# Optimization experiments

Measured on AMD Instinct MI355X. Metric: run time of the kernel, lower is better.

Reference implementation:

```python
import jax, jax.numpy as jnp
import numpy as np


def setup_inputs() -> dict:
    key = jax.random.key(0)
    k1, k2, k3, k4 = jax.random.split(key, 4)
    B, N, F_in, F_out = 8, 2048, 256, 256
    inp = jax.random.normal(k1, (B, N, F_in), dtype=jnp.float32)
    adj = jax.random.uniform(k2, (B, N, N), dtype=jnp.float32)
    stdv = 1.0 / np.sqrt(F_out)
    weight = jax.random.uniform(k3, (F_in, F_out), dtype=jnp.float32, minval=-stdv, maxval=stdv)
    bias = jax.random.uniform(k4, (F_out,), dtype=jnp.float32, minval=-stdv, maxval=stdv)
    return {"input": inp, "adj": adj, "weight": weight, "bias": bias}


def reference(input, adj, weight, bias):
    # d = (sum over dim 1 of adj) ** -0.5, matching torch adj.sum(dim=1)
    d = adj.sum(axis=1) ** -0.5  # [B, N]
    # D @ A @ D with diagonal D -> row/col broadcast scaling (same math)
    adj_norm = d[:, :, None] * adj * d[:, None, :]  # [B, N, N]
    support = jnp.einsum('bnf,fo->bno', input, weight)  # [B, N, F_out]
    output = jnp.einsum('bnm,bmo->bno', adj_norm, support) + bias
    return output
```

## Files before the change

kernel.cpp:

```cpp
#include <hip/hip_runtime.h>
#include <hip/hip_bf16.h>

#define BATCH 8
#define NDIM 2048
#define FDIM 256
#define CH 32

typedef float f32x4 __attribute__((ext_vector_type(4)));
typedef short bf16x8 __attribute__((ext_vector_type(8)));
typedef short bf16x4 __attribute__((ext_vector_type(4)));

__device__ __forceinline__ short f2bf(float f) {
  __hip_bfloat16 h = __float2bfloat16(f);
  short s;
  __builtin_memcpy(&s, &h, 2);
  return s;
}

__device__ __forceinline__ void gload_lds16(const void* g, void* l) {
  __builtin_amdgcn_global_load_lds(
      (const __attribute__((address_space(1))) void*)g,
      (__attribute__((address_space(3))) void*)l, 16, 0, 0);
}

__device__ __forceinline__ int aswz(int c, int r) {
  return 2 * ((c >> 1) ^ (r & 7)) + ((c & 1) ^ ((r >> 3) & 1));
}

__global__ __launch_bounds__(256) void k_colsum(const float* __restrict__ adj,
                                                float* __restrict__ part,
                                                const float* __restrict__ w,
                                                short* __restrict__ wt) {
  int bid = blockIdx.x;
  int t = threadIdx.x;
  if (bid < 512) {
    int cb = bid & 1;
    int ch = (bid >> 1) & (CH - 1);
    int b = bid >> 6;
    int col = cb * 1024 + t * 4;
    const float* p = adj + (size_t)b * NDIM * NDIM + (size_t)(ch * 64) * NDIM + col;
    f32x4 acc = {0.f, 0.f, 0.f, 0.f};
#pragma unroll 8
    for (int i = 0; i < 64; ++i) acc += *(const f32x4*)(p + (size_t)i * NDIM);
    *(f32x4*)(part + (size_t)(b * CH + ch) * NDIM + col) = acc;
  } else {
    __shared__ float tile[64][65];
    int bb = bid - 512;
    int bx = bb & 3, by = bb >> 2;
    int f0 = by * 64, o0 = bx * 64;
    int c4 = 4 * (t & 15);
#pragma unroll
    for (int q = 0; q < 4; ++q) {
      int r = (t >> 4) + 16 * q;
      f32x4 v = *(const f32x4*)(w + (size_t)(f0 + r) * FDIM + o0 + c4);
#pragma unroll
      for (int i = 0; i < 4; ++i) tile[r][c4 + i] = v[i];
    }
    __syncthreads();
#pragma unroll
    for (int q = 0; q < 4; ++q) {
      int r = (t >> 4) + 16 * q;
      bf16x4 pk;
#pragma unroll
      for (int i = 0; i < 4; ++i) pk[i] = f2bf(tile[c4 + i][r]);
      *(bf16x4*)(wt + (size_t)(o0 + r) * FDIM + f0 + c4) = pk;
    }
  }
}

__global__ __launch_bounds__(512) void k_support(const float* __restrict__ in,
                                                 const short* __restrict__ wt,
                                                 const float* __restrict__ part,
                                                 float* __restrict__ dnorm,
                                                 short* __restrict__ st) {
  __shared__ float Alf[3][64 * 64];
  __shared__ short Bl[3][256 * 64];
  __shared__ float dnLds[64];
  int t = threadIdx.x, lane = t & 63, w = t >> 6;
  int wm = w & 1, wn = w >> 1;
  int b = blockIdx.x & 7;
  int m0 = (blockIdx.x >> 3) * 64;
  const float* inb = in + ((size_t)b * NDIM + m0) * FDIM;

  if (t < 64) {
    float s = 0.f;
#pragma unroll
    for (int c = 0; c < CH; ++c) s += part[(size_t)(b * CH + c) * NDIM + m0 + t];
    float dv = rsqrtf(s);
    dnLds[t] = dv;
    dnorm[b * NDIM + m0 + t] = dv;
  }
  asm volatile("s_waitcnt vmcnt(0)" ::: "memory");

  int s0 = t, s1 = 512 + t;
  int r0 = s0 >> 4, c0 = aswz(s0 & 15, r0);
  int r1 = s1 >> 4, c1 = aswz(s1 & 15, r1);
  const float* a0s = inb + (size_t)r0 * FDIM + c0 * 4;
  const float* a1s = inb + (size_t)r1 * FDIM + c1 * 4;
  int arow = t >> 3;
  int schk = (t & 7) ^ (arow & 7);
  const short* bsrc = wt + (size_t)arow * FDIM + 8 * schk;

  f32x4 acc[2][4];
#pragma unroll
  for (int m = 0; m < 2; ++m)
#pragma unroll
    for (int n = 0; n < 4; ++n) acc[m][n] = {0.f, 0.f, 0.f, 0.f};

  int lr = lane & 15, kg = lane >> 4, sw = lane & 7;
  int bA = (lr >> 3) & 1;

  auto stage = [&](int k, int bp) {
    size_t ko = (size_t)k * 64;
    gload_lds16(a0s + ko, &Alf[bp][s0 * 4]);
    gload_lds16(a1s + ko, &Alf[bp][s1 * 4]);
#pragma unroll
    for (int i = 0; i < 4; ++i)
      gload_lds16(bsrc + (size_t)(i * 64) * FDIM + ko, &Bl[bp][(i * 512 + t) * 8]);
  };

  auto body = [&](int it, int bc, int bp, int mode) {
    if (mode == 0) {
      stage(it + 2, bp);
      asm volatile("s_waitcnt vmcnt(12)" ::: "memory");
    } else if (mode == 1) {
      asm volatile("s_waitcnt vmcnt(6)" ::: "memory");
    } else {
      asm volatile("s_waitcnt vmcnt(0)" ::: "memory");
    }
    __builtin_amdgcn_s_barrier();
    asm volatile("" ::: "memory");
    __builtin_amdgcn_sched_barrier(0);
#pragma unroll
    for (int h = 0; h < 2; ++h) {
      int gk = h * 4 + kg;
      int p2 = 2 * (gk ^ sw);
      bf16x8 af[2];
#pragma unroll
      for (int mf = 0; mf < 2; ++mf) {
        int row = wm * 32 + mf * 16 + lr;
        f32x4 lo = *(const f32x4*)&Alf[bc][row * 64 + (p2 + bA) * 4];
        f32x4 hi = *(const f32x4*)&Alf[bc][row * 64 + (p2 + (bA ^ 1)) * 4];
#pragma unroll
        for (int j = 0; j < 4; ++j) { af[mf][j] = f2bf(lo[j]); af[mf][4 + j] = f2bf(hi[j]); }
      }
      int kc = (gk ^ sw) * 8;
      bf16x8 bv0 = *(const bf16x8*)&Bl[bc][(wn * 64 + lr) * 64 + kc];
      bf16x8 bv1 = *(const bf16x8*)&Bl[bc][(wn * 64 + 16 + lr) * 64 + kc];
      bf16x8 bv2 = *(const bf16x8*)&Bl[bc][(wn * 64 + 32 + lr) * 64 + kc];
      bf16x8 bv3 = *(const bf16x8*)&Bl[bc][(wn * 64 + 48 + lr) * 64 + kc];
      acc[0][0] = __builtin_amdgcn_mfma_f32_16x16x32_bf16(af[0], bv0, acc[0][0], 0, 0, 0);
      acc[0][1] = __builtin_amdgcn_mfma_f32_16x16x32_bf16(af[0], bv1, acc[0][1], 0, 0, 0);
      acc[0][2] = __builtin_amdgcn_mfma_f32_16x16x32_bf16(af[0], bv2, acc[0][2], 0, 0, 0);
      acc[0][3] = __builtin_amdgcn_mfma_f32_16x16x32_bf16(af[0], bv3, acc[0][3], 0, 0, 0);
      acc[1][0] = __builtin_amdgcn_mfma_f32_16x16x32_bf16(af[1], bv0, acc[1][0], 0, 0, 0);
      acc[1][1] = __builtin_amdgcn_mfma_f32_16x16x32_bf16(af[1], bv1, acc[1][1], 0, 0, 0);
      acc[1][2] = __builtin_amdgcn_mfma_f32_16x16x32_bf16(af[1], bv2, acc[1][2], 0, 0, 0);
      acc[1][3] = __builtin_amdgcn_mfma_f32_16x16x32_bf16(af[1], bv3, acc[1][3], 0, 0, 0);
    }
    asm volatile("s_waitcnt lgkmcnt(0)" ::: "memory");
    __builtin_amdgcn_s_barrier();
    asm volatile("" ::: "memory");
  };

  stage(0, 0);
  stage(1, 1);
  body(0, 0, 2, 0);
  body(1, 1, 0, 0);
  body(2, 2, 1, 1);
  body(3, 0, 2, 2);

#pragma unroll
  for (int mf = 0; mf < 2; ++mf) {
    int rloc = wm * 32 + mf * 16 + kg * 4;
    int row = m0 + rloc;
    float dm[4];
#pragma unroll
    for (int j = 0; j < 4; ++j) dm[j] = dnLds[rloc + j];
#pragma unroll
    for (int nf = 0; nf < 4; ++nf) {
      int col = wn * 64 + nf * 16 + lr;
      bf16x4 pk;
#pragma unroll
      for (int j = 0; j < 4; ++j) pk[j] = f2bf(acc[mf][nf][j] * dm[j]);
      *(bf16x4*)(st + ((size_t)(b * FDIM + col)) * NDIM + row) = pk;
    }
  }
}

__global__ __launch_bounds__(512) void k_main(const float* __restrict__ adj,
                                              const short* __restrict__ st,
                                              const float* __restrict__ dnorm,
                                              const float* __restrict__ bias,
                                              float* __restrict__ out) {
  __shared__ float Alf[3][64 * 64];
  __shared__ short Bl[3][256 * 64];
  int t = threadIdx.x, lane = t & 63, w = t >> 6;
  int wm = w & 1, wn = w >> 1;
  int b = blockIdx.x & 7;
  int n0 = (blockIdx.x >> 3) * 64;
  const float* ab = adj + ((size_t)b * NDIM + n0) * NDIM;
  const short* stb = st + (size_t)b * FDIM * NDIM;

  int s0 = t, s1 = 512 + t;
  int r0 = s0 >> 4, c0 = aswz(s0 & 15, r0);
  int r1 = s1 >> 4, c1 = aswz(s1 & 15, r1);
  const float* a0s = ab + (size_t)r0 * NDIM + c0 * 4;
  const float* a1s = ab + (size_t)r1 * NDIM + c1 * 4;
  int arow = t >> 3;
  int schk = (t & 7) ^ (arow & 7);
  const short* bsrc = stb + (size_t)arow * NDIM + 8 * schk;

  f32x4 acc[2][4];
#pragma unroll
  for (int m = 0; m < 2; ++m)
#pragma unroll
    for (int n = 0; n < 4; ++n) acc[m][n] = {0.f, 0.f, 0.f, 0.f};

  int lr = lane & 15, kg = lane >> 4, sw = lane & 7;
  int bA = (lr >> 3) & 1;

  auto stage = [&](int k, int bp) {
    size_t ko = (size_t)k * 64;
    gload_lds16(a0s + ko, &Alf[bp][s0 * 4]);
    gload_lds16(a1s + ko, &Alf[bp][s1 * 4]);
#pragma unroll
    for (int i = 0; i < 4; ++i)
      gload_lds16(bsrc + (size_t)(i * 64) * NDIM + ko, &Bl[bp][(i * 512 + t) * 8]);
  };

  auto body = [&](int it, int bc, int bp, int mode) {
    if (mode == 0) {
      stage(it + 2, bp);
      asm volatile("s_waitcnt vmcnt(12)" ::: "memory");
    } else if (mode == 1) {
      asm volatile("s_waitcnt vmcnt(6)" ::: "memory");
    } else {
      asm volatile("s_waitcnt vmcnt(0)" ::: "memory");
    }
    __builtin_amdgcn_s_barrier();
    asm volatile("" ::: "memory");
    __builtin_amdgcn_sched_barrier(0);
#pragma unroll
    for (int h = 0; h < 2; ++h) {
      int gk = h * 4 + kg;
      int p2 = 2 * (gk ^ sw);
      bf16x8 af[2];
#pragma unroll
      for (int mf = 0; mf < 2; ++mf) {
        int row = wm * 32 + mf * 16 + lr;
        f32x4 lo = *(const f32x4*)&Alf[bc][row * 64 + (p2 + bA) * 4];
        f32x4 hi = *(const f32x4*)&Alf[bc][row * 64 + (p2 + (bA ^ 1)) * 4];
#pragma unroll
        for (int j = 0; j < 4; ++j) { af[mf][j] = f2bf(lo[j]); af[mf][4 + j] = f2bf(hi[j]); }
      }
      int kc = (gk ^ sw) * 8;
      bf16x8 bv0 = *(const bf16x8*)&Bl[bc][(wn * 64 + lr) * 64 + kc];
      bf16x8 bv1 = *(const bf16x8*)&Bl[bc][(wn * 64 + 16 + lr) * 64 + kc];
      bf16x8 bv2 = *(const bf16x8*)&Bl[bc][(wn * 64 + 32 + lr) * 64 + kc];
      bf16x8 bv3 = *(const bf16x8*)&Bl[bc][(wn * 64 + 48 + lr) * 64 + kc];
      acc[0][0] = __builtin_amdgcn_mfma_f32_16x16x32_bf16(af[0], bv0, acc[0][0], 0, 0, 0);
      acc[0][1] = __builtin_amdgcn_mfma_f32_16x16x32_bf16(af[0], bv1, acc[0][1], 0, 0, 0);
      acc[0][2] = __builtin_amdgcn_mfma_f32_16x16x32_bf16(af[0], bv2, acc[0][2], 0, 0, 0);
      acc[0][3] = __builtin_amdgcn_mfma_f32_16x16x32_bf16(af[0], bv3, acc[0][3], 0, 0, 0);
      acc[1][0] = __builtin_amdgcn_mfma_f32_16x16x32_bf16(af[1], bv0, acc[1][0], 0, 0, 0);
      acc[1][1] = __builtin_amdgcn_mfma_f32_16x16x32_bf16(af[1], bv1, acc[1][1], 0, 0, 0);
      acc[1][2] = __builtin_amdgcn_mfma_f32_16x16x32_bf16(af[1], bv2, acc[1][2], 0, 0, 0);
      acc[1][3] = __builtin_amdgcn_mfma_f32_16x16x32_bf16(af[1], bv3, acc[1][3], 0, 0, 0);
    }
    asm volatile("s_waitcnt lgkmcnt(0)" ::: "memory");
    __builtin_amdgcn_s_barrier();
    asm volatile("" ::: "memory");
  };

  stage(0, 0);
  stage(1, 1);
  for (int itb = 0; itb < 30; itb += 3) {
    body(itb + 0, 0, 2, 0);
    body(itb + 1, 1, 0, 0);
    body(itb + 2, 2, 1, 0);
  }
  body(30, 0, 2, 1);
  body(31, 1, 0, 2);

#pragma unroll
  for (int mf = 0; mf < 2; ++mf) {
    int row = n0 + wm * 32 + mf * 16 + kg * 4;
    f32x4 dr = *(const f32x4*)&dnorm[b * NDIM + row];
#pragma unroll
    for (int nf = 0; nf < 4; ++nf) {
      int col = wn * 64 + nf * 16 + lr;
      float bv = bias[col];
      float* op = out + ((size_t)b * NDIM + row) * FDIM + col;
#pragma unroll
      for (int j = 0; j < 4; ++j) op[(size_t)j * FDIM] = dr[j] * acc[mf][nf][j] + bv;
    }
  }
}

extern "C" void kernel_launch(void* const* d_in, const int* in_sizes, int n_in,
                              void* d_out, int out_size, void* d_ws, size_t ws_size,
                              hipStream_t stream) {
  (void)in_sizes; (void)n_in; (void)out_size; (void)ws_size;
  const float* input = (const float*)d_in[0];
  const float* adj = (const float*)d_in[1];
  const float* weight = (const float*)d_in[2];
  const float* bias = (const float*)d_in[3];
  float* out = (float*)d_out;

  char* ws = (char*)d_ws;
  short* st = (short*)ws;
  float* dnorm = (float*)(ws + 8ull * 1024 * 1024);
  float* part = (float*)(ws + 8ull * 1024 * 1024 + 65536);
  short* wt = (short*)(ws + 8ull * 1024 * 1024 + 65536 + 2ull * 1024 * 1024);

  k_colsum<<<dim3(528), dim3(256), 0, stream>>>(adj, part, weight, wt);
  k_support<<<dim3(BATCH * (NDIM / 64)), dim3(512), 0, stream>>>(input, wt, part, dnorm, st);
  k_main<<<dim3(BATCH * (NDIM / 64)), dim3(512), 0, stream>>>(adj, st, dnorm, bias, out);
}
```

Measured before the change: 70.48 us.

## Fuse column-sum, support GEMM and main GEMM into one kernel with per-batch barriers

The column-sum, support GEMM and main GEMM launches are merged into one 256-block kernel. A small init kernel transposes the weight and resets the counters. Each block first column-sums its own 64 rows of adj, then waits at an atomic-counter barrier per batch. It then computes its 64-row support tile and waits at a second barrier before running the main adj×support GEMM, keeping the degree normalisation in LDS. This removes launch gaps and the global dnorm round trip, and the colsum read of adj may warm caches for the main pass. In exchange, correctness depends on all 256 blocks being resident at once, and blocks spin while waiting.

```diff
diff --git a/kernel.cpp b/kernel.cpp
--- a/kernel.cpp
+++ b/kernel.cpp
@@ -27,52 +27,44 @@
   return 2 * ((c >> 1) ^ (r & 7)) + ((c & 1) ^ ((r >> 3) & 1));
 }
 
-__global__ __launch_bounds__(256) void k_colsum(const float* __restrict__ adj,
-                                                float* __restrict__ part,
-                                                const float* __restrict__ w,
-                                                short* __restrict__ wt) {
-  int bid = blockIdx.x;
+__global__ __launch_bounds__(256) void k_init(const float* __restrict__ w,
+                                              short* __restrict__ wt,
+                                              unsigned* __restrict__ ctr) {
   int t = threadIdx.x;
-  if (bid < 512) {
-    int cb = bid & 1;
-    int ch = (bid >> 1) & (CH - 1);
-    int b = bid >> 6;
-    int col = cb * 1024 + t * 4;
-    const float* p = adj + (size_t)b * NDIM * NDIM + (size_t)(ch * 64) * NDIM + col;
-    f32x4 acc = {0.f, 0.f, 0.f, 0.f};
-#pragma unroll 8
-    for (int i = 0; i < 64; ++i) acc += *(const f32x4*)(p + (size_t)i * NDIM);
-    *(f32x4*)(part + (size_t)(b * CH + ch) * NDIM + col) = acc;
-  } else {
-    __shared__ float tile[64][65];
-    int bb = bid - 512;
-    int bx = bb & 3, by = bb >> 2;
-    int f0 = by * 64, o0 = bx * 64;
-    int c4 = 4 * (t & 15);
-#pragma unroll
-    for (int q = 0; q < 4; ++q) {
-      int r = (t >> 4) + 16 * q;
-      f32x4 v = *(const f32x4*)(w + (size_t)(f0 + r) * FDIM + o0 + c4);
-#pragma unroll
-      for (int i = 0; i < 4; ++i) tile[r][c4 + i] = v[i];
-    }
-    __syncthreads();
-#pragma unroll
-    for (int q = 0; q < 4; ++q) {
-      int r = (t >> 4) + 16 * q;
-      bf16x4 pk;
-#pragma unroll
-      for (int i = 0; i < 4; ++i) pk[i] = f2bf(tile[c4 + i][r]);
-      *(bf16x4*)(wt + (size_t)(o0 + r) * FDIM + f0 + c4) = pk;
-    }
-  }
-}
-
-__global__ __launch_bounds__(512) void k_support(const float* __restrict__ in,
-                                                 const short* __restrict__ wt,
-                                                 const float* __restrict__ part,
-                                                 float* __restrict__ dnorm,
-                                                 short* __restrict__ st) {
+  if (blockIdx.x == 0) {
+    if (t < 16) ctr[t] = 0u;
+    return;
+  }
+  __shared__ float tile[64][65];
+  int bb = blockIdx.x - 1;
+  int bx = bb & 3, by = bb >> 2;
+  int f0 = by * 64, o0 = bx * 64;
+  int c4 = 4 * (t & 15);
+#pragma unroll
+  for (int q = 0; q < 4; ++q) {
+    int r = (t >> 4) + 16 * q;
+    f32x4 v = *(const f32x4*)(w + (size_t)(f0 + r) * FDIM + o0 + c4);
+#pragma unroll
+    for (int i = 0; i < 4; ++i) tile[r][c4 + i] = v[i];
+  }
+  __syncthreads();
+#pragma unroll
+  for (int q = 0; q < 4; ++q) {
+    int r = (t >> 4) + 16 * q;
+    bf16x4 pk;
+#pragma unroll
+    for (int i = 0; i < 4; ++i) pk[i] = f2bf(tile[c4 + i][r]);
+    *(bf16x4*)(wt + (size_t)(o0 + r) * FDIM + f0 + c4) = pk;
+  }
+}
+
+__global__ __launch_bounds__(512) void k_fused(const float* __restrict__ adj,
+                                               const float* __restrict__ in,
+                                               const short* __restrict__ wt,
+                                               float* __restrict__ part,
+                                               const float* __restrict__ bias,
+                                               float* __restrict__ out,
+                                               unsigned* __restrict__ ctr) {
   __shared__ float Alf[3][64 * 64];
   __shared__ short Bl[3][256 * 64];
   __shared__ float dnLds[64];
@@ -80,220 +72,232 @@
   int wm = w & 1, wn = w >> 1;
   int b = blockIdx.x & 7;
   int m0 = (blockIdx.x >> 3) * 64;
-  const float* inb = in + ((size_t)b * NDIM + m0) * FDIM;
-
-  if (t < 64) {
-    float s = 0.f;
-#pragma unroll
-    for (int c = 0; c < CH; ++c) s += part[(size_t)(b * CH + c) * NDIM + m0 + t];
-    float dv = rsqrtf(s);
-    dnLds[t] = dv;
-    dnorm[b * NDIM + m0 + t] = dv;
-  }
-  asm volatile("s_waitcnt vmcnt(0)" ::: "memory");
-
+  unsigned* ctrA = ctr;
+  unsigned* ctrB = ctr + 8;
+
+  {
+    int col = t * 4;
+    const float* p = adj + (size_t)b * NDIM * NDIM + (size_t)m0 * NDIM + col;
+    f32x4 acc = {0.f, 0.f, 0.f, 0.f};
+#pragma unroll 8
+    for (int i = 0; i < 64; ++i) acc += *(const f32x4*)(p + (size_t)i * NDIM);
+    *(f32x4*)(part + (size_t)(b * CH + (m0 >> 6)) * NDIM + col) = acc;
+  }
+  __threadfence();
+  __syncthreads();
+  if (t == 0) {
+    __hip_atomic_fetch_add(&ctrA[b], 1u, __ATOMIC_ACQ_REL, __HIP_MEMORY_SCOPE_AGENT);
+    while (__hip_atomic_load(&ctrA[b], __ATOMIC_ACQUIRE, __HIP_MEMORY_SCOPE_AGENT) < 32u)
+      __builtin_amdgcn_s_sleep(4);
+  }
+  __syncthreads();
+  __threadfence();
+
+  int lr = lane & 15, kg = lane >> 4, sw = lane & 7;
+  int bA = (lr >> 3) & 1;
   int s0 = t, s1 = 512 + t;
   int r0 = s0 >> 4, c0 = aswz(s0 & 15, r0);
   int r1 = s1 >> 4, c1 = aswz(s1 & 15, r1);
-  const float* a0s = inb + (size_t)r0 * FDIM + c0 * 4;
-  const float* a1s = inb + (size_t)r1 * FDIM + c1 * 4;
   int arow = t >> 3;
   int schk = (t & 7) ^ (arow & 7);
-  const short* bsrc = wt + (size_t)arow * FDIM + 8 * schk;
-
-  f32x4 acc[2][4];
-#pragma unroll
-  for (int m = 0; m < 2; ++m)
-#pragma unroll
-    for (int n = 0; n < 4; ++n) acc[m][n] = {0.f, 0.f, 0.f, 0.f};
-
-  int lr = lane & 15, kg = lane >> 4, sw = lane & 7;
-  int bA = (lr >> 3) & 1;
-
-  auto stage = [&](int k, int bp) {
-    size_t ko = (size_t)k * 64;
-    gload_lds16(a0s + ko, &Alf[bp][s0 * 4]);
-    gload_lds16(a1s + ko, &Alf[bp][s1 * 4]);
-#pragma unroll
-    for (int i = 0; i < 4; ++i)
-      gload_lds16(bsrc + (size_t)(i * 64) * FDIM + ko, &Bl[bp][(i * 512 + t) * 8]);
-  };
-
-  auto body = [&](int it, int bc, int bp, int mode) {
-    if (mode == 0) {
-      stage(it + 2, bp);
-      asm volatile("s_waitcnt vmcnt(12)" ::: "memory");
-    } else if (mode == 1) {
-      asm volatile("s_waitcnt vmcnt(6)" ::: "memory");
-    } else {
-      asm volatile("s_waitcnt vmcnt(0)" ::: "memory");
+
+  {
+    if (t < 64) {
+      float s = 0.f;
+#pragma unroll
+      for (int c = 0; c < CH; ++c) s += part[(size_t)(b * CH + c) * NDIM + m0 + t];
+      dnLds[t] = rsqrtf(s);
     }
-    __builtin_amdgcn_s_barrier();
-    asm volatile("" ::: "memory");
-    __builtin_amdgcn_sched_barrier(0);
-#pragma unroll
-    for (int h = 0; h < 2; ++h) {
-      int gk = h * 4 + kg;
-      int p2 = 2 * (gk ^ sw);
-      bf16x8 af[2];
-#pragma unroll
-      for (int mf = 0; mf < 2; ++mf) {
-        int row = wm * 32 + mf * 16 + lr;
-        f32x4 lo = *(const f32x4*)&Alf[bc][row * 64 + (p2 + bA) * 4];
-        f32x4 hi = *(const f32x4*)&Alf[bc][row * 64 + (p2 + (bA ^ 1)) * 4];
-#pragma unroll
-        for (int j = 0; j < 4; ++j) { af[mf][j] = f2bf(lo[j]); af[mf][4 + j] = f2bf(hi[j]); }
-      }
-      int kc = (gk ^ sw) * 8;
-      bf16x8 bv0 = *(const bf16x8*)&Bl[bc][(wn * 64 + lr) * 64 + kc];
-      bf16x8 bv1 = *(const bf16x8*)&Bl[bc][(wn * 64 + 16 + lr) * 64 + kc];
-      bf16x8 bv2 = *(const bf16x8*)&Bl[bc][(wn * 64 + 32 + lr) * 64 + kc];
-      bf16x8 bv3 = *(const bf16x8*)&Bl[bc][(wn * 64 + 48 + lr) * 64 + kc];
-      acc[0][0] = __builtin_amdgcn_mfma_f32_16x16x32_bf16(af[0], bv0, acc[0][0], 0, 0, 0);
-      acc[0][1] = __builtin_amdgcn_mfma_f32_16x16x32_bf16(af[0], bv1, acc[0][1], 0, 0, 0);
-      acc[0][2] = __builtin_amdgcn_mfma_f32_16x16x32_bf16(af[0], bv2, acc[0][2], 0, 0, 0);
-      acc[0][3] = __builtin_amdgcn_mfma_f32_16x16x32_bf16(af[0], bv3, acc[0][3], 0, 0, 0);
-      acc[1][0] = __builtin_amdgcn_mfma_f32_16x16x32_bf16(af[1], bv0, acc[1][0], 0, 0, 0);
-      acc[1][1] = __builtin_amdgcn_mfma_f32_16x16x32_bf16(af[1], bv1, acc[1][1], 0, 0, 0);
-      acc[1][2] = __builtin_amdgcn_mfma_f32_16x16x32_bf16(af[1], bv2, acc[1][2], 0, 0, 0);
-      acc[1][3] = __builtin_amdgcn_mfma_f32_16x16x32_bf16(af[1], bv3, acc[1][3], 0, 0, 0);
+    asm volatile("s_waitcnt vmcnt(0)" ::: "memory");
+
+    const float* inb = in + ((size_t)b * NDIM + m0) * FDIM;
+    const float* a0s = inb + (size_t)r0 * FDIM + c0 * 4;
+    const float* a1s = inb + (size_t)r1 * FDIM + c1 * 4;
+    const short* bsrc = wt + (size_t)arow * FDIM + 8 * schk;
+    short* st = (short*)nullptr;
+    st = (short*)((char*)part - (8ull * 1024 * 1024 + 65536));
+
+    f32x4 acc[2][4];
+#pragma unroll
+    for (int m = 0; m < 2; ++m)
+#pragma unroll
+      for (int n = 0; n < 4; ++n) acc[m][n] = {0.f, 0.f, 0.f, 0.f};
+
+    auto stage = [&](int k, int bp) {
+      size_t ko = (size_t)k * 64;
+      gload_lds16(a0s + ko, &Alf[bp][s0 * 4]);
+      gload_lds16(a1s + ko, &Alf[bp][s1 * 4]);
+#pragma unroll
+      for (int i = 0; i < 4; ++i)
+        gload_lds16(bsrc + (size_t)(i * 64) * FDIM + ko, &Bl[bp][(i * 512 + t) * 8]);
+    };
+    auto body = [&](int bc, int bp, int mode, int itp2) {
+      if (mode == 0) {
+        stage(itp2, bp);
+        asm volatile("s_waitcnt vmcnt(12)" ::: "memory");
+      } else if (mode == 1) {
+        asm volatile("s_waitcnt vmcnt(6)" ::: "memory");
+      } else {
+        asm volatile("s_waitcnt vmcnt(0)" ::: "memory");
+      }
+      __builtin_amdgcn_s_barrier();
+      asm volatile("" ::: "memory");
+      __builtin_amdgcn_sched_barrier(0);
+#pragma unroll
+      for (int h = 0; h < 2; ++h) {
+        int gk = h * 4 + kg;
+        int p2 = 2 * (gk ^ sw);
+        bf16x8 af[2];
+#pragma unroll
+        for (int mf = 0; mf < 2; ++mf) {
+          int row = wm * 32 + mf * 16 + lr;
+          f32x4 lo = *(const f32x4*)&Alf[bc][row * 64 + (p2 + bA) * 4];
+          f32x4 hi = *(const f32x4*)&Alf[bc][row * 64 + (p2 + (bA ^ 1)) * 4];
+#pragma unroll
+          for (int j = 0; j < 4; ++j) { af[mf][j] = f2bf(lo[j]); af[mf][4 + j] = f2bf(hi[j]); }
+        }
+        int kc = (gk ^ sw) * 8;
+        bf16x8 bv0 = *(const bf16x8*)&Bl[bc][(wn * 64 + lr) * 64 + kc];
+        bf16x8 bv1 = *(const bf16x8*)&Bl[bc][(wn * 64 + 16 + lr) * 64 + kc];
+        bf16x8 bv2 = *(const bf16x8*)&Bl[bc][(wn * 64 + 32 + lr) * 64 + kc];
+        bf16x8 bv3 = *(const bf16x8*)&Bl[bc][(wn * 64 + 48 + lr) * 64 + kc];
+        acc[0][0] = __builtin_amdgcn_mfma_f32_16x16x32_bf16(af[0], bv0, acc[0][0], 0, 0, 0);
+        acc[0][1] = __builtin_amdgcn_mfma_f32_16x16x32_bf16(af[0], bv1, acc[0][1], 0, 0, 0);
+        acc[0][2] = __builtin_amdgcn_mfma_f32_16x16x32_bf16(af[0], bv2, acc[0][2], 0, 0, 0);
+        acc[0][3] = __builtin_amdgcn_mfma_f32_16x16x32_bf16(af[0], bv3, acc[0][3], 0, 0, 0);
+        acc[1][0] = __builtin_amdgcn_mfma_f32_16x16x32_bf16(af[1], bv0, acc[1][0], 0, 0, 0);
+        acc[1][1] = __builtin_amdgcn_mfma_f32_16x16x32_bf16(af[1], bv1, acc[1][1], 0, 0, 0);
+        acc[1][2] = __builtin_amdgcn_mfma_f32_16x16x32_bf16(af[1], bv2, acc[1][2], 0, 0, 0);
+        acc[1][3] = __builtin_amdgcn_mfma_f32_16x16x32_bf16(af[1], bv3, acc[1][3], 0, 0, 0);
+      }
+      asm volatile("s_waitcnt lgkmcnt(0)" ::: "memory");
+      __builtin_amdgcn_s_barrier();
+      asm volatile("" ::: "memory");
+    };
+
+    stage(0, 0);
+    stage(1, 1);
+    body(0, 2, 0, 2);
+    body(1, 0, 0, 3);
+    body(2, 1, 1, 0);
+    body(0, 2, 2, 0);
+
+#pragma unroll
+    for (int mf = 0; mf < 2; ++mf) {
+      int rloc = wm * 32 + mf * 16 + kg * 4;
+      int row = m0 + rloc;
+      float dm[4];
+#pragma unroll
+      for (int j = 0; j < 4; ++j) dm[j] = dnLds[rloc + j];
+#pragma unroll
+      for (int nf = 0; nf < 4; ++nf) {
+        int col = wn * 64 + nf * 16 + lr;
+        bf16x4 pk;
+#pragma unroll
+        for (int j = 0; j < 4; ++j) pk[j] = f2bf(acc[mf][nf][j] * dm[j]);
+        *(bf16x4*)(st + ((size_t)(b * FDIM + col)) * NDIM + row) = pk;
+      }
     }
-    asm volatile("s_waitcnt lgkmcnt(0)" ::: "memory");
-    __builtin_amdgcn_s_barrier();
-    asm volatile("" ::: "memory");
-  };
-
-  stage(0, 0);
-  stage(1, 1);
-  body(0, 0, 2, 0);
-  body(1, 1, 0, 0);
-  body(2, 2, 1, 1);
-  body(3, 0, 2, 2);
-
-#pragma unroll
-  for (int mf = 0; mf < 2; ++mf) {
-    int rloc = wm * 32 + mf * 16 + kg * 4;
-    int row = m0 + rloc;
-    float dm[4];
-#pragma unroll
-    for (int j = 0; j < 4; ++j) dm[j] = dnLds[rloc + j];
-#pragma unroll
-    for (int nf = 0; nf < 4; ++nf) {
-      int col = wn * 64 + nf * 16 + lr;
-      bf16x4 pk;
-#pragma unroll
-      for (int j = 0; j < 4; ++j) pk[j] = f2bf(acc[mf][nf][j] * dm[j]);
-      *(bf16x4*)(st + ((size_t)(b * FDIM + col)) * NDIM + row) = pk;
+  }
+  __threadfence();
+  __syncthreads();
+  if (t == 0) {
+    __hip_atomic_fetch_add(&ctrB[b], 1u, __ATOMIC_ACQ_REL, __HIP_MEMORY_SCOPE_AGENT);
+    while (__hip_atomic_load(&ctrB[b], __ATOMIC_ACQUIRE, __HIP_MEMORY_SCOPE_AGENT) < 32u)
+      __builtin_amdgcn_s_sleep(4);
+  }
+  __syncthreads();
+  __threadfence();
+
+  {
+    const short* st = (const short*)((char*)part - (8ull * 1024 * 1024 + 65536));
+    const float* ab = adj + ((size_t)b * NDIM + m0) * NDIM;
+    const short* stb = st + (size_t)b * FDIM * NDIM;
+    const float* a0s = ab + (size_t)r0 * NDIM + c0 * 4;
+    const float* a1s = ab + (size_t)r1 * NDIM + c1 * 4;
+    const short* bsrc = stb + (size_t)arow * NDIM + 8 * schk;
+
+    f32x4 acc[2][4];
+#pragma unroll
+    for (int m = 0; m < 2; ++m)
+#pragma unroll
+      for (int n = 0; n < 4; ++n) acc[m][n] = {0.f, 0.f, 0.f, 0.f};
+
+    auto stage = [&](int k, int bp) {
+      size_t ko = (size_t)k * 64;
+      gload_lds16(a0s + ko, &Alf[bp][s0 * 4]);
+      gload_lds16(a1s + ko, &Alf[bp][s1 * 4]);
+#pragma unroll
+      for (int i = 0; i < 4; ++i)
+        gload_lds16(bsrc + (size_t)(i * 64) * NDIM + ko, &Bl[bp][(i * 512 + t) * 8]);
+    };
+    auto body = [&](int it, int bc, int bp, int mode) {
+      if (mode == 0) {
+        stage(it + 2, bp);
+        asm volatile("s_waitcnt vmcnt(12)" ::: "memory");
+      } else if (mode == 1) {
+        asm volatile("s_waitcnt vmcnt(6)" ::: "memory");
+      } else {
+        asm volatile("s_waitcnt vmcnt(0)" ::: "memory");
+      }
+      __builtin_amdgcn_s_barrier();
+      asm volatile("" ::: "memory");
+      __builtin_amdgcn_sched_barrier(0);
+#pragma unroll
+      for (int h = 0; h < 2; ++h) {
+        int gk = h * 4 + kg;
+        int p2 = 2 * (gk ^ sw);
+        bf16x8 af[2];
+#pragma unroll
+        for (int mf = 0; mf < 2; ++mf) {
+          int row = wm * 32 + mf * 16 + lr;
+          f32x4 lo = *(const f32x4*)&Alf[bc][row * 64 + (p2 + bA) * 4];
+          f32x4 hi = *(const f32x4*)&Alf[bc][row * 64 + (p2 + (bA ^ 1)) * 4];
+#pragma unroll
+          for (int j = 0; j < 4; ++j) { af[mf][j] = f2bf(lo[j]); af[mf][4 + j] = f2bf(hi[j]); }
+        }
+        int kc = (gk ^ sw) * 8;
+        bf16x8 bv0 = *(const bf16x8*)&Bl[bc][(wn * 64 + lr) * 64 + kc];
+        bf16x8 bv1 = *(const bf16x8*)&Bl[bc][(wn * 64 + 16 + lr) * 64 + kc];
+        bf16x8 bv2 = *(const bf16x8*)&Bl[bc][(wn * 64 + 32 + lr) * 64 + kc];
+        bf16x8 bv3 = *(const bf16x8*)&Bl[bc][(wn * 64 + 48 + lr) * 64 + kc];
+        acc[0][0] = __builtin_amdgcn_mfma_f32_16x16x32_bf16(af[0], bv0, acc[0][0], 0, 0, 0);
+        acc[0][1] = __builtin_amdgcn_mfma_f32_16x16x32_bf16(af[0], bv1, acc[0][1], 0, 0, 0);
+        acc[0][2] = __builtin_amdgcn_mfma_f32_16x16x32_bf16(af[0], bv2, acc[0][2], 0, 0, 0);
+        acc[0][3] = __builtin_amdgcn_mfma_f32_16x16x32_bf16(af[0], bv3, acc[0][3], 0, 0, 0);
+        acc[1][0] = __builtin_amdgcn_mfma_f32_16x16x32_bf16(af[1], bv0, acc[1][0], 0, 0, 0);
+        acc[1][1] = __builtin_amdgcn_mfma_f32_16x16x32_bf16(af[1], bv1, acc[1][1], 0, 0, 0);
+        acc[1][2] = __builtin_amdgcn_mfma_f32_16x16x32_bf16(af[1], bv2, acc[1][2], 0, 0, 0);
+        acc[1][3] = __builtin_amdgcn_mfma_f32_16x16x32_bf16(af[1], bv3, acc[1][3], 0, 0, 0);
+      }
+      asm volatile("s_waitcnt lgkmcnt(0)" ::: "memory");
+      __builtin_amdgcn_s_barrier();
+      asm volatile("" ::: "memory");
+    };
+
+    stage(0, 0);
+    stage(1, 1);
+    for (int itb = 0; itb < 30; itb += 3) {
+      body(itb + 0, 0, 2, 0);
+      body(itb + 1, 1, 0, 0);
+      body(itb + 2, 2, 1, 0);
     }
-  }
-}
-
-__global__ __launch_bounds__(512) void k_main(const float* __restrict__ adj,
-                                              const short* __restrict__ st,
-                                              const float* __restrict__ dnorm,
-                                              const float* __restrict__ bias,
-                                              float* __restrict__ out) {
-  __shared__ float Alf[3][64 * 64];
-  __shared__ short Bl[3][256 * 64];
-  int t = threadIdx.x, lane = t & 63, w = t >> 6;
-  int wm = w & 1, wn = w >> 1;
-  int b = blockIdx.x & 7;
-  int n0 = (blockIdx.x >> 3) * 64;
-  const float* ab = adj + ((size_t)b * NDIM + n0) * NDIM;
-  const short* stb = st + (size_t)b * FDIM * NDIM;
-
-  int s0 = t, s1 = 512 + t;
-  int r0 = s0 >> 4, c0 = aswz(s0 & 15, r0);
-  int r1 = s1 >> 4, c1 = aswz(s1 & 15, r1);
-  const float* a0s = ab + (size_t)r0 * NDIM + c0 * 4;
-  const float* a1s = ab + (size_t)r1 * NDIM + c1 * 4;
-  int arow = t >> 3;
-  int schk = (t & 7) ^ (arow & 7);
-  const short* bsrc = stb + (size_t)arow * NDIM + 8 * schk;
-
-  f32x4 acc[2][4];
-#pragma unroll
-  for (int m = 0; m < 2; ++m)
-#pragma unroll
-    for (int n = 0; n < 4; ++n) acc[m][n] = {0.f, 0.f, 0.f, 0.f};
-
-  int lr = lane & 15, kg = lane >> 4, sw = lane & 7;
-  int bA = (lr >> 3) & 1;
-
-  auto stage = [&](int k, int bp) {
-    size_t ko = (size_t)k * 64;
-    gload_lds16(a0s + ko, &Alf[bp][s0 * 4]);
-    gload_lds16(a1s + ko, &Alf[bp][s1 * 4]);
-#pragma unroll
-    for (int i = 0; i < 4; ++i)
-      gload_lds16(bsrc + (size_t)(i * 64) * NDIM + ko, &Bl[bp][(i * 512 + t) * 8]);
-  };
-
-  auto body = [&](int it, int bc, int bp, int mode) {
-    if (mode == 0) {
-      stage(it + 2, bp);
-      asm volatile("s_waitcnt vmcnt(12)" ::: "memory");
-    } else if (mode == 1) {
-      asm volatile("s_waitcnt vmcnt(6)" ::: "memory");
-    } else {
-      asm volatile("s_waitcnt vmcnt(0)" ::: "memory");
-    }
-    __builtin_amdgcn_s_barrier();
-    asm volatile("" ::: "memory");
-    __builtin_amdgcn_sched_barrier(0);
-#pragma unroll
-    for (int h = 0; h < 2; ++h) {
-      int gk = h * 4 + kg;
-      int p2 = 2 * (gk ^ sw);
-      bf16x8 af[2];
-#pragma unroll
-      for (int mf = 0; mf < 2; ++mf) {
-        int row = wm * 32 + mf * 16 + lr;
-        f32x4 lo = *(const f32x4*)&Alf[bc][row * 64 + (p2 + bA) * 4];
-        f32x4 hi = *(const f32x4*)&Alf[bc][row * 64 + (p2 + (bA ^ 1)) * 4];
-#pragma unroll
-        for (int j = 0; j < 4; ++j) { af[mf][j] = f2bf(lo[j]); af[mf][4 + j] = f2bf(hi[j]); }
-      }
-      int kc = (gk ^ sw) * 8;
-      bf16x8 bv0 = *(const bf16x8*)&Bl[bc][(wn * 64 + lr) * 64 + kc];
-      bf16x8 bv1 = *(const bf16x8*)&Bl[bc][(wn * 64 + 16 + lr) * 64 + kc];
-      bf16x8 bv2 = *(const bf16x8*)&Bl[bc][(wn * 64 + 32 + lr) * 64 + kc];
-      bf16x8 bv3 = *(const bf16x8*)&Bl[bc][(wn * 64 + 48 + lr) * 64 + kc];
-      acc[0][0] = __builtin_amdgcn_mfma_f32_16x16x32_bf16(af[0], bv0, acc[0][0], 0, 0, 0);
-      acc[0][1] = __builtin_amdgcn_mfma_f32_16x16x32_bf16(af[0], bv1, acc[0][1], 0, 0, 0);
-      acc[0][2] = __builtin_amdgcn_mfma_f32_16x16x32_bf16(af[0], bv2, acc[0][2], 0, 0, 0);
-      acc[0][3] = __builtin_amdgcn_mfma_f32_16x16x32_bf16(af[0], bv3, acc[0][3], 0, 0, 0);
-      acc[1][0] = __builtin_amdgcn_mfma_f32_16x16x32_bf16(af[1], bv0, acc[1][0], 0, 0, 0);
-      acc[1][1] = __builtin_amdgcn_mfma_f32_16x16x32_bf16(af[1], bv1, acc[1][1], 0, 0, 0);
-      acc[1][2] = __builtin_amdgcn_mfma_f32_16x16x32_bf16(af[1], bv2, acc[1][2], 0, 0, 0);
-      acc[1][3] = __builtin_amdgcn_mfma_f32_16x16x32_bf16(af[1], bv3, acc[1][3], 0, 0, 0);
-    }
-    asm volatile("s_waitcnt lgkmcnt(0)" ::: "memory");
-    __builtin_amdgcn_s_barrier();
-    asm volatile("" ::: "memory");
-  };
-
-  stage(0, 0);
-  stage(1, 1);
-  for (int itb = 0; itb < 30; itb += 3) {
-    body(itb + 0, 0, 2, 0);
-    body(itb + 1, 1, 0, 0);
-    body(itb + 2, 2, 1, 0);
-  }
-  body(30, 0, 2, 1);
-  body(31, 1, 0, 2);
-
-#pragma unroll
-  for (int mf = 0; mf < 2; ++mf) {
-    int row = n0 + wm * 32 + mf * 16 + kg * 4;
-    f32x4 dr = *(const f32x4*)&dnorm[b * NDIM + row];
-#pragma unroll
-    for (int nf = 0; nf < 4; ++nf) {
-      int col = wn * 64 + nf * 16 + lr;
-      float bv = bias[col];
-      float* op = out + ((size_t)b * NDIM + row) * FDIM + col;
-#pragma unroll
-      for (int j = 0; j < 4; ++j) op[(size_t)j * FDIM] = dr[j] * acc[mf][nf][j] + bv;
+    body(30, 0, 2, 1);
+    body(31, 1, 0, 2);
+
+#pragma unroll
+    for (int mf = 0; mf < 2; ++mf) {
+      int rloc = wm * 32 + mf * 16 + kg * 4;
+      int row = m0 + rloc;
+      f32x4 dr = *(const f32x4*)&dnLds[rloc];
+#pragma unroll
+      for (int nf = 0; nf < 4; ++nf) {
+        int col = wn * 64 + nf * 16 + lr;
+        float bv = bias[col];
+        float* op = out + ((size_t)b * NDIM + row) * FDIM + col;
+#pragma unroll
+        for (int j = 0; j < 4; ++j) op[(size_t)j * FDIM] = dr[j] * acc[mf][nf][j] + bv;
+      }
     }
   }
 }
@@ -309,12 +313,10 @@
   float* out = (float*)d_out;
 
   char* ws = (char*)d_ws;
-  short* st = (short*)ws;
-  float* dnorm = (float*)(ws + 8ull * 1024 * 1024);
   float* part = (float*)(ws + 8ull * 1024 * 1024 + 65536);
   short* wt = (short*)(ws + 8ull * 1024 * 1024 + 65536 + 2ull * 1024 * 1024);
-
-  k_colsum<<<dim3(528), dim3(256), 0, stream>>>(adj, part, weight, wt);
-  k_support<<<dim3(BATCH * (NDIM / 64)), dim3(512), 0, stream>>>(input, wt, part, dnorm, st);
-  k_main<<<dim3(BATCH * (NDIM / 64)), dim3(512), 0, stream>>>(adj, st, dnorm, bias, out);
-}
+  unsigned* ctr = (unsigned*)(ws + 16ull * 1024 * 1024);
+
+  k_init<<<dim3(17), dim3(256), 0, stream>>>(weight, wt, ctr);
+  k_fused<<<dim3(256), dim3(512), 0, stream>>>(adj, input, wt, part, bias, out, ctr);
+}
```

Result: slower. 260.9 us (+270.2%).

## Fuse colsum, support GEMM and main GEMM into one cooperative persistent kernel

Applied to the files above, without the earlier changes.

Replaces the three-kernel sequence with a small init kernel (weight transpose plus counter reset) and a single cooperative kernel of 256 blocks. Each block computes its own column-sum partial, then its slice of the support GEMM, then its tile of the main GEMM, and uses per-batch atomic-counter barriers between phases instead of kernel boundaries. This removes launch gaps and tail effects between kernels, and the adj slab read for the colsum may still be in cache when the main phase reads it. It depends on every block being co-resident, relies on spin-wait barriers, and falls back to the old launches if the cooperative launch fails.

```diff
diff --git a/kernel.cpp b/kernel.cpp
--- a/kernel.cpp
+++ b/kernel.cpp
@@ -25,6 +25,279 @@
 
 __device__ __forceinline__ int aswz(int c, int r) {
   return 2 * ((c >> 1) ^ (r & 7)) + ((c & 1) ^ ((r >> 3) & 1));
+}
+
+__global__ __launch_bounds__(256) void k_init(const float* __restrict__ w,
+                                              short* __restrict__ wt,
+                                              unsigned* __restrict__ ctr) {
+  int t = threadIdx.x;
+  if (blockIdx.x == 0) {
+    for (int i = t; i < 512; i += 256) ctr[i] = 0u;
+    return;
+  }
+  __shared__ float tile[64][65];
+  int bb = blockIdx.x - 1;
+  int bx = bb & 3, by = bb >> 2;
+  int f0 = by * 64, o0 = bx * 64;
+  int c4 = 4 * (t & 15);
+#pragma unroll
+  for (int q = 0; q < 4; ++q) {
+    int r = (t >> 4) + 16 * q;
+    f32x4 v = *(const f32x4*)(w + (size_t)(f0 + r) * FDIM + o0 + c4);
+#pragma unroll
+    for (int i = 0; i < 4; ++i) tile[r][c4 + i] = v[i];
+  }
+  __syncthreads();
+#pragma unroll
+  for (int q = 0; q < 4; ++q) {
+    int r = (t >> 4) + 16 * q;
+    bf16x4 pk;
+#pragma unroll
+    for (int i = 0; i < 4; ++i) pk[i] = f2bf(tile[c4 + i][r]);
+    *(bf16x4*)(wt + (size_t)(o0 + r) * FDIM + f0 + c4) = pk;
+  }
+}
+
+__global__ __launch_bounds__(512) void k_fused(const float* __restrict__ adj,
+                                               const float* __restrict__ in,
+                                               const short* __restrict__ wt,
+                                               float* __restrict__ part,
+                                               short* __restrict__ st,
+                                               const float* __restrict__ bias,
+                                               float* __restrict__ out,
+                                               unsigned* __restrict__ ctr) {
+  __shared__ float Alf[3][64 * 64];
+  __shared__ short Bl[3][256 * 64];
+  __shared__ float dnLds[64];
+  int t = threadIdx.x, lane = t & 63, w = t >> 6;
+  int wm = w & 1, wn = w >> 1;
+  int b = blockIdx.x & 7;
+  int m0 = (blockIdx.x >> 3) * 64;
+
+  {
+    int col = t * 4;
+    const float* p = adj + (size_t)b * NDIM * NDIM + (size_t)m0 * NDIM + col;
+    f32x4 acc = {0.f, 0.f, 0.f, 0.f};
+#pragma unroll 8
+    for (int i = 0; i < 64; ++i) acc += *(const f32x4*)(p + (size_t)i * NDIM);
+    *(f32x4*)(part + (size_t)(b * CH + (m0 >> 6)) * NDIM + col) = acc;
+  }
+  __threadfence();
+  __syncthreads();
+  if (t == 0) {
+    unsigned* c = &ctr[b * 32];
+    __hip_atomic_fetch_add(c, 1u, __ATOMIC_ACQ_REL, __HIP_MEMORY_SCOPE_AGENT);
+    while (__hip_atomic_load(c, __ATOMIC_ACQUIRE, __HIP_MEMORY_SCOPE_AGENT) < 32u)
+      __builtin_amdgcn_s_sleep(16);
+  }
+  __syncthreads();
+  __threadfence();
+
+  int lr = lane & 15, kg = lane >> 4, sw = lane & 7;
+  int bA = (lr >> 3) & 1;
+  int s0 = t, s1 = 512 + t;
+  int r0 = s0 >> 4, c0 = aswz(s0 & 15, r0);
+  int r1 = s1 >> 4, c1 = aswz(s1 & 15, r1);
+  int arow = t >> 3;
+  int schk = (t & 7) ^ (arow & 7);
+
+  {
+    if (t < 64) {
+      float s = 0.f;
+#pragma unroll
+      for (int c = 0; c < CH; ++c) s += part[(size_t)(b * CH + c) * NDIM + m0 + t];
+      dnLds[t] = rsqrtf(s);
+    }
+    asm volatile("s_waitcnt vmcnt(0)" ::: "memory");
+
+    const float* inb = in + ((size_t)b * NDIM + m0) * FDIM;
+    const float* a0s = inb + (size_t)r0 * FDIM + c0 * 4;
+    const float* a1s = inb + (size_t)r1 * FDIM + c1 * 4;
+    const short* bsrc = wt + (size_t)arow * FDIM + 8 * schk;
+
+    f32x4 acc[2][4];
+#pragma unroll
+    for (int m = 0; m < 2; ++m)
+#pragma unroll
+      for (int n = 0; n < 4; ++n) acc[m][n] = {0.f, 0.f, 0.f, 0.f};
+
+    auto stage = [&](int k, int bp) {
+      size_t ko = (size_t)k * 64;
+      gload_lds16(a0s + ko, &Alf[bp][s0 * 4]);
+      gload_lds16(a1s + ko, &Alf[bp][s1 * 4]);
+#pragma unroll
+      for (int i = 0; i < 4; ++i)
+        gload_lds16(bsrc + (size_t)(i * 64) * FDIM + ko, &Bl[bp][(i * 512 + t) * 8]);
+    };
+    auto body = [&](int bc, int bp, int mode, int itp2) {
+      if (mode == 0) {
+        stage(itp2, bp);
+        asm volatile("s_waitcnt vmcnt(12)" ::: "memory");
+      } else if (mode == 1) {
+        asm volatile("s_waitcnt vmcnt(6)" ::: "memory");
+      } else {
+        asm volatile("s_waitcnt vmcnt(0)" ::: "memory");
+      }
+      __builtin_amdgcn_s_barrier();
+      asm volatile("" ::: "memory");
+      __builtin_amdgcn_sched_barrier(0);
+#pragma unroll
+      for (int h = 0; h < 2; ++h) {
+        int gk = h * 4 + kg;
+        int p2 = 2 * (gk ^ sw);
+        bf16x8 af[2];
+#pragma unroll
+        for (int mf = 0; mf < 2; ++mf) {
+          int row = wm * 32 + mf * 16 + lr;
+          f32x4 lo = *(const f32x4*)&Alf[bc][row * 64 + (p2 + bA) * 4];
+          f32x4 hi = *(const f32x4*)&Alf[bc][row * 64 + (p2 + (bA ^ 1)) * 4];
+#pragma unroll
+          for (int j = 0; j < 4; ++j) { af[mf][j] = f2bf(lo[j]); af[mf][4 + j] = f2bf(hi[j]); }
+        }
+        int kc = (gk ^ sw) * 8;
+        bf16x8 bv0 = *(const bf16x8*)&Bl[bc][(wn * 64 + lr) * 64 + kc];
+        bf16x8 bv1 = *(const bf16x8*)&Bl[bc][(wn * 64 + 16 + lr) * 64 + kc];
+        bf16x8 bv2 = *(const bf16x8*)&Bl[bc][(wn * 64 + 32 + lr) * 64 + kc];
+        bf16x8 bv3 = *(const bf16x8*)&Bl[bc][(wn * 64 + 48 + lr) * 64 + kc];
+        acc[0][0] = __builtin_amdgcn_mfma_f32_16x16x32_bf16(af[0], bv0, acc[0][0], 0, 0, 0);
+        acc[0][1] = __builtin_amdgcn_mfma_f32_16x16x32_bf16(af[0], bv1, acc[0][1], 0, 0, 0);
+        acc[0][2] = __builtin_amdgcn_mfma_f32_16x16x32_bf16(af[0], bv2, acc[0][2], 0, 0, 0);
+        acc[0][3] = __builtin_amdgcn_mfma_f32_16x16x32_bf16(af[0], bv3, acc[0][3], 0, 0, 0);
+        acc[1][0] = __builtin_amdgcn_mfma_f32_16x16x32_bf16(af[1], bv0, acc[1][0], 0, 0, 0);
+        acc[1][1] = __builtin_amdgcn_mfma_f32_16x16x32_bf16(af[1], bv1, acc[1][1], 0, 0, 0);
+        acc[1][2] = __builtin_amdgcn_mfma_f32_16x16x32_bf16(af[1], bv2, acc[1][2], 0, 0, 0);
+        acc[1][3] = __builtin_amdgcn_mfma_f32_16x16x32_bf16(af[1], bv3, acc[1][3], 0, 0, 0);
+      }
+      asm volatile("s_waitcnt lgkmcnt(0)" ::: "memory");
+      __builtin_amdgcn_s_barrier();
+      asm volatile("" ::: "memory");
+    };
+
+    stage(0, 0);
+    stage(1, 1);
+    body(0, 2, 0, 2);
+    body(1, 0, 0, 3);
+    body(2, 1, 1, 0);
+    body(0, 2, 2, 0);
+
+#pragma unroll
+    for (int mf = 0; mf < 2; ++mf) {
+      int rloc = wm * 32 + mf * 16 + kg * 4;
+      int row = m0 + rloc;
+      float dm[4];
+#pragma unroll
+      for (int j = 0; j < 4; ++j) dm[j] = dnLds[rloc + j];
+#pragma unroll
+      for (int nf = 0; nf < 4; ++nf) {
+        int col = wn * 64 + nf * 16 + lr;
+        bf16x4 pk;
+#pragma unroll
+        for (int j = 0; j < 4; ++j) pk[j] = f2bf(acc[mf][nf][j] * dm[j]);
+        *(bf16x4*)(st + ((size_t)(b * FDIM + col)) * NDIM + row) = pk;
+      }
+    }
+  }
+  __threadfence();
+  __syncthreads();
+  if (t == 0) {
+    unsigned* c = &ctr[256 + b * 32];
+    __hip_atomic_fetch_add(c, 1u, __ATOMIC_ACQ_REL, __HIP_MEMORY_SCOPE_AGENT);
+    while (__hip_atomic_load(c, __ATOMIC_ACQUIRE, __HIP_MEMORY_SCOPE_AGENT) < 32u)
+      __builtin_amdgcn_s_sleep(16);
+  }
+  __syncthreads();
+  __threadfence();
+
+  {
+    const float* ab = adj + ((size_t)b * NDIM + m0) * NDIM;
+    const short* stb = st + (size_t)b * FDIM * NDIM;
+    const float* a0s = ab + (size_t)r0 * NDIM + c0 * 4;
+    const float* a1s = ab + (size_t)r1 * NDIM + c1 * 4;
+    const short* bsrc = stb + (size_t)arow * NDIM + 8 * schk;
+
+    f32x4 acc[2][4];
+#pragma unroll
+    for (int m = 0; m < 2; ++m)
+#pragma unroll
+      for (int n = 0; n < 4; ++n) acc[m][n] = {0.f, 0.f, 0.f, 0.f};
+
+    auto stage = [&](int k, int bp) {
+      size_t ko = (size_t)k * 64;
+      gload_lds16(a0s + ko, &Alf[bp][s0 * 4]);
+      gload_lds16(a1s + ko, &Alf[bp][s1 * 4]);
+#pragma unroll
+      for (int i = 0; i < 4; ++i)
+        gload_lds16(bsrc + (size_t)(i * 64) * NDIM + ko, &Bl[bp][(i * 512 + t) * 8]);
+    };
+    auto body = [&](int it, int bc, int bp, int mode) {
+      if (mode == 0) {
+        stage(it + 2, bp);
+        asm volatile("s_waitcnt vmcnt(12)" ::: "memory");
+      } else if (mode == 1) {
+        asm volatile("s_waitcnt vmcnt(6)" ::: "memory");
+      } else {
+        asm volatile("s_waitcnt vmcnt(0)" ::: "memory");
+      }
+      __builtin_amdgcn_s_barrier();
+      asm volatile("" ::: "memory");
+      __builtin_amdgcn_sched_barrier(0);
+#pragma unroll
+      for (int h = 0; h < 2; ++h) {
+        int gk = h * 4 + kg;
+        int p2 = 2 * (gk ^ sw);
+        bf16x8 af[2];
+#pragma unroll
+        for (int mf = 0; mf < 2; ++mf) {
+          int row = wm * 32 + mf * 16 + lr;
+          f32x4 lo = *(const f32x4*)&Alf[bc][row * 64 + (p2 + bA) * 4];
+          f32x4 hi = *(const f32x4*)&Alf[bc][row * 64 + (p2 + (bA ^ 1)) * 4];
+#pragma unroll
+          for (int j = 0; j < 4; ++j) { af[mf][j] = f2bf(lo[j]); af[mf][4 + j] = f2bf(hi[j]); }
+        }
+        int kc = (gk ^ sw) * 8;
+        bf16x8 bv0 = *(const bf16x8*)&Bl[bc][(wn * 64 + lr) * 64 + kc];
+        bf16x8 bv1 = *(const bf16x8*)&Bl[bc][(wn * 64 + 16 + lr) * 64 + kc];
+        bf16x8 bv2 = *(const bf16x8*)&Bl[bc][(wn * 64 + 32 + lr) * 64 + kc];
+        bf16x8 bv3 = *(const bf16x8*)&Bl[bc][(wn * 64 + 48 + lr) * 64 + kc];
+        acc[0][0] = __builtin_amdgcn_mfma_f32_16x16x32_bf16(af[0], bv0, acc[0][0], 0, 0, 0);
+        acc[0][1] = __builtin_amdgcn_mfma_f32_16x16x32_bf16(af[0], bv1, acc[0][1], 0, 0, 0);
+        acc[0][2] = __builtin_amdgcn_mfma_f32_16x16x32_bf16(af[0], bv2, acc[0][2], 0, 0, 0);
+        acc[0][3] = __builtin_amdgcn_mfma_f32_16x16x32_bf16(af[0], bv3, acc[0][3], 0, 0, 0);
+        acc[1][0] = __builtin_amdgcn_mfma_f32_16x16x32_bf16(af[1], bv0, acc[1][0], 0, 0, 0);
+        acc[1][1] = __builtin_amdgcn_mfma_f32_16x16x32_bf16(af[1], bv1, acc[1][1], 0, 0, 0);
+        acc[1][2] = __builtin_amdgcn_mfma_f32_16x16x32_bf16(af[1], bv2, acc[1][2], 0, 0, 0);
+        acc[1][3] = __builtin_amdgcn_mfma_f32_16x16x32_bf16(af[1], bv3, acc[1][3], 0, 0, 0);
+      }
+      asm volatile("s_waitcnt lgkmcnt(0)" ::: "memory");
+      __builtin_amdgcn_s_barrier();
+      asm volatile("" ::: "memory");
+    };
+
+    stage(0, 0);
+    stage(1, 1);
+    for (int itb = 0; itb < 30; itb += 3) {
+      body(itb + 0, 0, 2, 0);
+      body(itb + 1, 1, 0, 0);
+      body(itb + 2, 2, 1, 0);
+    }
+    body(30, 0, 2, 1);
+    body(31, 1, 0, 2);
+
+#pragma unroll
+    for (int mf = 0; mf < 2; ++mf) {
+      int rloc = wm * 32 + mf * 16 + kg * 4;
+      int row = m0 + rloc;
+      f32x4 dr = *(const f32x4*)&dnLds[rloc];
+#pragma unroll
+      for (int nf = 0; nf < 4; ++nf) {
+        int col = wn * 64 + nf * 16 + lr;
+        float bv = bias[col];
+        float* op = out + ((size_t)b * NDIM + row) * FDIM + col;
+#pragma unroll
+        for (int j = 0; j < 4; ++j) op[(size_t)j * FDIM] = dr[j] * acc[mf][nf][j] + bv;
+      }
+    }
+  }
 }
 
 __global__ __launch_bounds__(256) void k_colsum(const float* __restrict__ adj,
@@ -118,7 +391,6 @@
     for (int i = 0; i < 4; ++i)
       gload_lds16(bsrc + (size_t)(i * 64) * FDIM + ko, &Bl[bp][(i * 512 + t) * 8]);
   };
-
   auto body = [&](int it, int bc, int bp, int mode) {
     if (mode == 0) {
       stage(it + 2, bp);
@@ -228,7 +500,6 @@
     for (int i = 0; i < 4; ++i)
       gload_lds16(bsrc + (size_t)(i * 64) * NDIM + ko, &Bl[bp][(i * 512 + t) * 8]);
   };
-
   auto body = [&](int it, int bc, int bp, int mode) {
     if (mode == 0) {
       stage(it + 2, bp);
@@ -313,8 +584,18 @@
   float* dnorm = (float*)(ws + 8ull * 1024 * 1024);
   float* part = (float*)(ws + 8ull * 1024 * 1024 + 65536);
   short* wt = (short*)(ws + 8ull * 1024 * 1024 + 65536 + 2ull * 1024 * 1024);
-
-  k_colsum<<<dim3(528), dim3(256), 0, stream>>>(adj, part, weight, wt);
-  k_support<<<dim3(BATCH * (NDIM / 64)), dim3(512), 0, stream>>>(input, wt, part, dnorm, st);
-  k_main<<<dim3(BATCH * (NDIM / 64)), dim3(512), 0, stream>>>(adj, st, dnorm, bias, out);
-}
+  unsigned* ctr = (unsigned*)(ws + 16ull * 1024 * 1024);
+
+  k_init<<<dim3(17), dim3(256), 0, stream>>>(weight, wt, ctr);
+
+  void* kargs[] = {(void*)&adj, (void*)&input, (void*)&wt, (void*)&part,
+                   (void*)&st, (void*)&bias, (void*)&out, (void*)&ctr};
+  hipError_t e = hipLaunchCooperativeKernel((const void*)k_fused, dim3(256),
+                                            dim3(512), kargs, 0, stream);
+  if (e != hipSuccess) {
+    (void)hipGetLastError();
+    k_colsum<<<dim3(528), dim3(256), 0, stream>>>(adj, part, weight, wt);
+    k_support<<<dim3(256), dim3(512), 0, stream>>>(input, wt, part, dnorm, st);
+    k_main<<<dim3(256), dim3(512), 0, stream>>>(adj, st, dnorm, bias, out);
+  }
+}
```

Result: slower. 263.5 us (+273.9%).
